# Optimization experiments

Hardware: AMD Instinct MI355X
Metric: run time of the kernel (lower is better)

Reference implementation:

```python
import jax, jax.numpy as jnp
import numpy as np

B, T, DIN, DOUT = 64, 128, 32, 64
HE, HD, K = 512, 1024, 12
NPH, NPL = 512, 64
# per-sample decoder parameter layout: Whh, bh, Wih, C, D
_PSI_SHAPES = [(HD, HD), (HD,), (DIN, HD), (HD, DOUT), (DIN, DOUT - DIN)]
_PSI_SIZES = [int(np.prod(s)) for s in _PSI_SHAPES]
_PSI_OFF = np.cumsum([0] + _PSI_SIZES)
NPSI = int(_PSI_OFF[-1])


def _xavier(key, shape):
    fan_in, fan_out = shape[-2], shape[-1]
    lim = np.sqrt(6.0 / (fan_in + fan_out))
    return jax.random.uniform(key, shape, jnp.float32, -lim, lim)


def setup_inputs() -> dict:
    key = jax.random.key(0)
    ks = jax.random.split(key, 16)
    gru_bias = jnp.concatenate([jnp.zeros(HD), jnp.ones(HD)])  # z-gate bias init to 1
    return {
        'inputs': jax.random.normal(ks[0], (B, T, DIN), jnp.float32),
        'outputs': jax.random.normal(ks[1], (B, T, DOUT), jnp.float32),
        'eps': jax.random.normal(ks[2], (B, K), jnp.float32),
        'state': jnp.zeros((B, HD), jnp.float32),
        'enc_Wih': _xavier(ks[3], (3 * HE, DOUT)),
        'enc_Whh': _xavier(ks[4], (3 * HE, HE)),
        'enc_bih': jnp.zeros(3 * HE, jnp.float32),
        'enc_bhh': jnp.zeros(3 * HE, jnp.float32),
        'to_mu': _xavier(ks[5], (HE, K)),
        'to_lsigma': _xavier(ks[6], (HE, K)),
        'to_lsigma_bias': -0.5 * jnp.ones(K, jnp.float32),
        'psi_W1': _xavier(ks[7], (K, NPH)),
        'psi_b1': jnp.zeros(NPH, jnp.float32),
        'psi_W2': _xavier(ks[8], (NPH, NPL)),
        'psi_b2': jnp.zeros(NPL, jnp.float32),
        'psi_W3': _xavier(ks[9], (NPL, NPSI)) * 0.05,
        'psi_b3': jnp.zeros(NPSI, jnp.float32),
        'gru_Wih': _xavier(ks[10], (DIN, 2 * HD)),
        'gru_Whh': _xavier(ks[11], (HD, 2 * HD)),
        'gru_bias': gru_bias,
    }


def _forward(inputs, outputs, eps, state, enc_Wih, enc_Whh, enc_bih, enc_bhh,
             to_mu, to_lsigma, to_lsigma_bias, psi_W1, psi_b1, psi_W2, psi_b2,
             psi_W3, psi_b3, gru_Wih, gru_Whh, gru_bias):
    # ---- encoder: shared GRUCell over time (torch GRUCell semantics) ----
    def enc_step(h, x):
        gi = x @ enc_Wih.T + enc_bih          # [B,3HE]
        gh = h @ enc_Whh.T + enc_bhh
        ir, iz, inn = jnp.split(gi, 3, axis=-1)
        hr, hz, hn = jnp.split(gh, 3, axis=-1)
        r = jax.nn.sigmoid(ir + hr)
        z = jax.nn.sigmoid(iz + hz)
        n = jnp.tanh(inn + r * hn)
        return (1.0 - z) * n + z * h, None
    h0 = jnp.zeros((outputs.shape[0], HE), outputs.dtype)
    h_enc, _ = jax.lax.scan(enc_step, h0, jnp.swapaxes(outputs, 0, 1))

    mu = h_enc @ to_mu
    logstd = h_enc @ to_lsigma + to_lsigma_bias
    z_lat = mu + eps * jnp.exp(logstd)

    # ---- hypernetwork: decode per-sample GRU params ----
    psi = (jnp.tanh(z_lat @ psi_W1 + psi_b1) @ psi_W2 + psi_b2) @ psi_W3 + psi_b3  # [B,NPSI]
    parts = [psi[:, _PSI_OFF[i]:_PSI_OFF[i + 1]].reshape((-1,) + _PSI_SHAPES[i])
             for i in range(5)]
    Whh_b, bh_b, Wih_b, C_b, D_b = parts

    # ---- per-sample partial GRU over time (batched via einsum) ----
    def dec_step(h, x):
        gx = x @ gru_Wih                       # [B,2HD] shared gates
        gh = h @ gru_Whh
        r = jax.nn.sigmoid(gx[:, :HD] + gh[:, :HD] + gru_bias[:HD])
        zt = jax.nn.sigmoid(gx[:, HD:] + gh[:, HD:] + gru_bias[HD:])
        eta = jnp.tanh(jnp.einsum('bi,bih->bh', x, Wih_b)
                       + r * jnp.einsum('bh,bhg->bg', h, Whh_b) + bh_b)
        h_new = zt * h + (1.0 - zt) * eta
        return h_new, h_new
    _, dec = jax.lax.scan(dec_step, state, jnp.swapaxes(inputs, 0, 1))
    dec = jnp.swapaxes(dec, 0, 1)              # [B,T,HD]

    # residual_output with HUMAN_SIZE > input_dim: concat(raw inputs, inputs@D)
    resid = jnp.concatenate([inputs, jnp.einsum('bti,bio->bto', inputs, D_b)], axis=-1)
    yhats = jnp.einsum('bth,bho->bto', dec, C_b) + resid
    states = jax.lax.stop_gradient(dec[:, -1, :])
    return yhats, mu, logstd, states


def reference(inputs, outputs, eps, state, enc_Wih, enc_Whh, enc_bih, enc_bhh,
              to_mu, to_lsigma, to_lsigma_bias, psi_W1, psi_b1, psi_W2, psi_b2,
              psi_W3, psi_b3, gru_Wih, gru_Whh, gru_bias):
    return _forward(inputs, outputs, eps, state, enc_Wih, enc_Whh, enc_bih, enc_bhh,
                    to_mu, to_lsigma, to_lsigma_bias, psi_W1, psi_b1, psi_W2, psi_b2,
                    psi_W3, psi_b3, gru_Wih, gru_Whh, gru_bias)
```

## Files before the change

kernel.cpp:

```cpp
#include <hip/hip_runtime.h>
#include <stdint.h>

#define B_ 64
#define T_ 128
#define DIN_ 32
#define DOUT_ 64
#define HE_ 512
#define HD_ 1024
#define NPSI_ 1148928
#define PPS_ 100352

typedef short bf16x8 __attribute__((ext_vector_type(8)));
typedef float f32x4 __attribute__((ext_vector_type(4)));
typedef int   i32x4 __attribute__((ext_vector_type(4)));

__device__ __forceinline__ unsigned short f2b(float f){
  unsigned u = __float_as_uint(f);
  u += 0x7fffu + ((u>>16)&1u);
  return (unsigned short)(u>>16);
}
__device__ __forceinline__ float b2f(unsigned short s){
  return __uint_as_float(((unsigned)s)<<16);
}
__device__ __forceinline__ float sigm_(float x){
  float e = __expf(-x);
  return 1.f/(1.f+e);
}
__device__ __forceinline__ float tanh_(float x){
  float e = __expf(2.f*x);
  return 1.f - 2.f/(e+1.f);
}
__device__ __forceinline__ void glds16(const void* g, void* l) {
  __builtin_amdgcn_global_load_lds(
      (const __attribute__((address_space(1))) unsigned int*)g,
      (__attribute__((address_space(3))) unsigned int*)l, 16, 0, 0);
}

__global__ __launch_bounds__(512) void k_prep(
    const float* __restrict__ enc_Whh, const float* __restrict__ enc_Wih,
    const float* __restrict__ gru_Whh, const float* __restrict__ state,
    unsigned short* __restrict__ encW_f, unsigned short* __restrict__ encI_f,
    unsigned short* __restrict__ gru_f, unsigned short* __restrict__ h_dec)
{
  int blk = blockIdx.x, tid = threadIdx.x;
  if (blk < 1536) {
    int nt = blk >> 4, kt = blk & 15;
    int c = tid >> 5, k = tid & 31;
    float v = enc_Whh[(size_t)(nt*16 + c)*HE_ + kt*32 + k];
    int l = c + ((k>>3)<<4), jj = k & 7;
    encW_f[(size_t)(nt*16 + kt)*512 + l*8 + jj] = f2b(v);
  } else if (blk < 1728) {
    int f = blk - 1536; int nt = f >> 1, kt = f & 1;
    int c = tid >> 5, k = tid & 31;
    float v = enc_Wih[(size_t)(nt*16 + c)*DOUT_ + kt*32 + k];
    int l = c + ((k>>3)<<4), jj = k & 7;
    encI_f[(size_t)(nt*2 + kt)*512 + l*8 + jj] = f2b(v);
  } else if (blk < 5824) {
    int f = blk - 1728; int nt = f >> 5, kt = f & 31;
    int k = tid >> 4, c = tid & 15;
    float v = gru_Whh[(size_t)(kt*32 + k)*2048 + nt*16 + c];
    int l = c + ((k>>3)<<4), jj = k & 7;
    gru_f[(size_t)(nt*32 + kt)*512 + l*8 + jj] = f2b(v);
  } else {
    int b = blk - 5824;
    h_dec[(size_t)b*HD_ + tid]       = f2b(state[(size_t)b*HD_ + tid]);
    h_dec[(size_t)b*HD_ + 512 + tid] = f2b(state[(size_t)b*HD_ + 512 + tid]);
  }
}

__global__ __launch_bounds__(128) void k_encoder(
    const float* __restrict__ outputs, const float* __restrict__ bih, const float* __restrict__ bhh,
    const unsigned short* __restrict__ encW_f, const unsigned short* __restrict__ encI_f,
    unsigned short* __restrict__ h_buf, float* __restrict__ h_enc, unsigned int* __restrict__ bar)
{
  __shared__ __align__(16) unsigned short h_bf[16*520];
  __shared__ __align__(16) unsigned short xa[16*72];
  __shared__ float part[64*16];
  int tid = threadIdx.x, wv = tid >> 6, lane = tid & 63;
  int g = blockIdx.x >> 5, bg = blockIdx.x & 31;
  int c0 = bg*16, gs = g*8;
  for (int i = tid; i < 16*520; i += 128) h_bf[i] = 0;
  for (int i = tid; i < 16*72; i += 128) xa[i] = 0;
  int cl = c0 + (lane & 15);
  float br_b = bih[cl] + bhh[cl];
  float bz_b = bih[512+cl] + bhh[512+cl];
  float bin_b = bih[1024+cl];
  float bhn_b = bhh[1024+cl];
  float hreg[4] = {0.f,0.f,0.f,0.f};
  int row = (lane>>4)<<2;
  int nt_r = bg, nt_z = 32+bg, nt_n = 64+bg;
  __syncthreads();
  for (int t = 0; t < 128; ++t) {
    int rb = t & 1;
    if (t > 0) {
      if (tid == 0) {
        while (__hip_atomic_load(&bar[(g<<7)+(t-1)], __ATOMIC_ACQUIRE, __HIP_MEMORY_SCOPE_AGENT) < 32u)
          __builtin_amdgcn_s_sleep(2);
      }
      __syncthreads();
    }
    {
      const unsigned short* src = h_buf + (size_t)rb*B_*HE_ + (size_t)gs*HE_;
      #pragma unroll
      for (int j = 0; j < 4; ++j) {
        int chunk = j*128 + tid;
        bf16x8 v = *(const bf16x8*)(src + chunk*8);
        int s = chunk >> 6, col = (chunk & 63) * 8;
        *(bf16x8*)(&h_bf[s*520 + col]) = v;
      }
      #pragma unroll
      for (int j = 0; j < 4; ++j) {
        int e = j*128 + tid;
        int s = e >> 6, d = e & 63;
        xa[s*72 + d] = f2b(outputs[((size_t)(gs+s)*T_ + t)*DOUT_ + d]);
      }
    }
    __syncthreads();
    f32x4 accr = {0,0,0,0}, accz = {0,0,0,0}, accn = {0,0,0,0}, accgi = {0,0,0,0};
    {
      bf16x8 a = *(const bf16x8*)(&xa[(lane&15)*72 + wv*32 + ((lane>>4)<<3)]);
      bf16x8 b0 = *(const bf16x8*)(encI_f + (size_t)(nt_r*2+wv)*512 + lane*8);
      bf16x8 b1 = *(const bf16x8*)(encI_f + (size_t)(nt_z*2+wv)*512 + lane*8);
      bf16x8 b2 = *(const bf16x8*)(encI_f + (size_t)(nt_n*2+wv)*512 + lane*8);
      accr  = __builtin_amdgcn_mfma_f32_16x16x32_bf16(a, b0, accr, 0,0,0);
      accz  = __builtin_amdgcn_mfma_f32_16x16x32_bf16(a, b1, accz, 0,0,0);
      accgi = __builtin_amdgcn_mfma_f32_16x16x32_bf16(a, b2, accgi, 0,0,0);
    }
    #pragma unroll
    for (int kk = 0; kk < 8; ++kk) {
      int kt = wv*8 + kk;
      bf16x8 a = *(const bf16x8*)(&h_bf[(lane&15)*520 + kt*32 + ((lane>>4)<<3)]);
      bf16x8 b0 = *(const bf16x8*)(encW_f + (size_t)(nt_r*16+kt)*512 + lane*8);
      bf16x8 b1 = *(const bf16x8*)(encW_f + (size_t)(nt_z*16+kt)*512 + lane*8);
      bf16x8 b2 = *(const bf16x8*)(encW_f + (size_t)(nt_n*16+kt)*512 + lane*8);
      accr = __builtin_amdgcn_mfma_f32_16x16x32_bf16(a, b0, accr, 0,0,0);
      accz = __builtin_amdgcn_mfma_f32_16x16x32_bf16(a, b1, accz, 0,0,0);
      accn = __builtin_amdgcn_mfma_f32_16x16x32_bf16(a, b2, accn, 0,0,0);
    }
    if (wv == 1) {
      #pragma unroll
      for (int i = 0; i < 4; ++i) {
        part[lane*16 + i]      = accr[i];
        part[lane*16 + 4 + i]  = accz[i];
        part[lane*16 + 8 + i]  = accn[i];
        part[lane*16 + 12 + i] = accgi[i];
      }
    }
    __syncthreads();
    if (wv == 0 && row < 8) {
      unsigned short* dst = h_buf + (size_t)(rb^1)*B_*HE_;
      #pragma unroll
      for (int i = 0; i < 4; ++i) {
        int s = row + i;
        float ar  = accr[i]  + part[lane*16 + i];
        float az  = accz[i]  + part[lane*16 + 4 + i];
        float an  = accn[i]  + part[lane*16 + 8 + i];
        float agi = accgi[i] + part[lane*16 + 12 + i];
        float r = sigm_(ar + br_b);
        float z = sigm_(az + bz_b);
        float n = tanh_(agi + bin_b + r*(an + bhn_b));
        float hn = (1.f - z)*n + z*hreg[i];
        hreg[i] = hn;
        dst[(size_t)(gs+s)*HE_ + cl] = f2b(hn);
        if (t == 127) h_enc[(size_t)(gs+s)*HE_ + cl] = hn;
      }
    }
    __syncthreads();
    if (tid == 0)
      __hip_atomic_fetch_add(&bar[(g<<7)+t], 1u, __ATOMIC_ACQ_REL, __HIP_MEMORY_SCOPE_AGENT);
  }
}

__global__ __launch_bounds__(64) void k_latent(
    const float* __restrict__ h_enc, const float* __restrict__ to_mu,
    const float* __restrict__ to_ls, const float* __restrict__ ls_bias,
    const float* __restrict__ eps, float* __restrict__ out_mu,
    float* __restrict__ out_ls, float* __restrict__ z_lat)
{
  __shared__ float hb[512];
  int b = blockIdx.x, tid = threadIdx.x;
  #pragma unroll
  for (int j = 0; j < 8; ++j) hb[j*64 + tid] = h_enc[(size_t)b*HE_ + j*64 + tid];
  __syncthreads();
  if (tid < 12) {
    float m = 0.f, s = 0.f;
    #pragma unroll 8
    for (int k = 0; k < 512; ++k) {
      float h = hb[k];
      m += h * to_mu[k*12 + tid];
      s += h * to_ls[k*12 + tid];
    }
    s += ls_bias[tid];
    out_mu[b*12 + tid] = m;
    out_ls[b*12 + tid] = s;
    z_lat[b*12 + tid] = m + eps[b*12 + tid] * __expf(s);
  }
}

__global__ __launch_bounds__(512) void k_hidden(
    const float* __restrict__ z_lat, const float* __restrict__ W1, const float* __restrict__ b1,
    const float* __restrict__ W2, const float* __restrict__ b2, float* __restrict__ hidden_T)
{
  __shared__ float zl[12];
  __shared__ float a[512];
  int b = blockIdx.x, tid = threadIdx.x;
  if (tid < 12) zl[tid] = z_lat[b*12 + tid];
  __syncthreads();
  float acc = b1[tid];
  #pragma unroll
  for (int k = 0; k < 12; ++k) acc += zl[k] * W1[k*512 + tid];
  a[tid] = tanh_(acc);
  __syncthreads();
  if (tid < 64) {
    float h = b2[tid];
    #pragma unroll 8
    for (int j = 0; j < 512; ++j) h += a[j] * W2[j*64 + tid];
    hidden_T[tid*64 + b] = h;
  }
}

__global__ __launch_bounds__(1024) void k_psi(
    const float* __restrict__ hidden_T, const float* __restrict__ W3, const float* __restrict__ b3,
    signed char* __restrict__ whh_q, float* __restrict__ scales, float* __restrict__ params)
{
  __shared__ float hid[64*64];
  __shared__ unsigned lmax[64];
  int tid = threadIdx.x, blk = blockIdx.x;
  if (tid < 64) lmax[tid] = 0;
  #pragma unroll
  for (int j = 0; j < 4; ++j) hid[j*1024 + tid] = hidden_T[j*1024 + tid];
  __syncthreads();
  float acc[64];
  size_t j; int i_loc = 0, c_loc = 0, kt = 0, cp = 0;
  bool is_whh = blk < 1024;
  if (is_whh) {
    kt = blk >> 5; cp = blk & 31;
    i_loc = tid >> 5; c_loc = tid & 31;
    j = (size_t)(kt*32 + i_loc)*1024 + cp*32 + c_loc;
  } else {
    j = (size_t)1048576 + (size_t)(blk - 1024)*1024 + tid;
  }
  float bv = b3[j];
  #pragma unroll
  for (int b = 0; b < 64; ++b) acc[b] = bv;
  for (int k = 0; k < 64; ++k) {
    float wv = W3[(size_t)k*NPSI_ + j];
    #pragma unroll
    for (int bq = 0; bq < 16; ++bq) {
      f32x4 h4 = *(const f32x4*)(&hid[k*64 + bq*4]);
      acc[bq*4+0] += wv * h4[0];
      acc[bq*4+1] += wv * h4[1];
      acc[bq*4+2] += wv * h4[2];
      acc[bq*4+3] += wv * h4[3];
    }
  }
  if (is_whh) {
    #pragma unroll
    for (int b = 0; b < 64; ++b)
      atomicMax(&lmax[b], __float_as_uint(fabsf(acc[b])));
    __syncthreads();
    int ct = cp*2 + (c_loc>>4);
    int l = (c_loc & 15) + (((i_loc>>3)&3)<<4);
    int jj = i_loc & 7;
    size_t base = ((size_t)ct*32 + (size_t)kt)*512 + l*8 + jj;
    #pragma unroll
    for (int b = 0; b < 64; ++b) {
      float m = __uint_as_float(lmax[b]);
      float inv = (m > 0.f) ? (127.f/m) : 0.f;
      int q = (int)rintf(acc[b]*inv);
      whh_q[(size_t)b*1048576 + base] = (signed char)q;
    }
    if (tid < 64)
      scales[(size_t)tid*1024 + kt*32 + cp] = __uint_as_float(lmax[tid]);
  } else {
    size_t off = j - 1048576;
    #pragma unroll
    for (int b = 0; b < 64; ++b)
      params[(size_t)b*PPS_ + off] = acc[b];
  }
}

__global__ __launch_bounds__(512, 2) void k_decoder(
    const float* __restrict__ inputs, const float* __restrict__ gru_Wih,
    const float* __restrict__ gru_bias,
    const signed char* __restrict__ whh_q, const float* __restrict__ scales,
    const unsigned short* __restrict__ gru_f, const float* __restrict__ params,
    unsigned short* __restrict__ h_buf, float* __restrict__ dec,
    float* __restrict__ out_states, unsigned int* __restrict__ bar)
{
  __shared__ __align__(16) unsigned short h_bf[8*1048];
  __shared__ __align__(16) signed char h_q8[8*1040];
  __shared__ __align__(16) char stg[8][2][6144];
  __shared__ unsigned short wih_lds[8192];
  __shared__ unsigned short gwih_lds[2048];
  __shared__ float x_lds[256];
  __shared__ float gh_lds[1024];
  __shared__ float mv_lds[256];
  __shared__ float sc_lds[256];
  int tid = threadIdx.x;
  int g = blockIdx.x >> 5, bg = blockIdx.x & 31;
  int c0 = bg*32, gs = g*8;
  int w = tid >> 6, lane = tid & 63;
  int s_t = (tid >> 5) & 7, c_t = tid & 31;
  int sg_t = gs + s_t, cg_t = c0 + c_t;
  float bh_r = 0.f, br_b = 0.f, bz_b = 0.f;
  if (tid < 256) {
    bh_r = params[(size_t)sg_t*PPS_ + cg_t];
    br_b = gru_bias[cg_t];
    bz_b = gru_bias[1024 + cg_t];
  }
  for (int idx = tid; idx < 2048; idx += 512) {
    int i = idx >> 6, gc = idx & 63;
    gwih_lds[idx] = f2b(gru_Wih[i*2048 + (gc>>5)*1024 + c0 + (gc&31)]);
  }
  for (int idx = tid; idx < 8192; idx += 512) {
    int s = idx >> 10, r = idx & 1023;
    wih_lds[idx] = f2b(params[(size_t)(gs+s)*PPS_ + 1024 + (r>>5)*1024 + c0 + (r&31)]);
  }
  if (lane < 32)
    sc_lds[w*32 + lane] = scales[(size_t)(gs+w)*1024 + lane*32 + bg] * (1.f/16129.f);
  const char* af0c = (const char*)whh_q + (size_t)((gs+w)*64 + 2*bg)*16384 + lane*16;
  const char* af1c = af0c + 16384;
  int j_t = w >> 1;
  int nt_j = (j_t < 2) ? (2*bg + j_t) : (64 + 2*bg + (j_t - 2));
  const char* gfc = (const char*)(gru_f + ((size_t)nt_j*32 + (w&1)*16)*512) + lane*16;
  int ho_l = (lane>>4)<<3;
  int ghk0 = (w&1)*16;
  char* bufA = &stg[w][0][0];
  char* bufB = &stg[w][1][0];

  auto ISSUE = [&](char* bufp, int cc) {
    const char* a0 = af0c + (size_t)cc*2048;
    const char* a1 = af1c + (size_t)cc*2048;
    const char* gg = gfc  + (size_t)cc*2048;
    glds16(a0,        bufp);        glds16(a0 + 1024, bufp + 1024);
    glds16(a1,        bufp + 2048); glds16(a1 + 1024, bufp + 3072);
    glds16(gg,        bufp + 4096); glds16(gg + 1024, bufp + 5120);
  };
  f32x4 agh, facc0, facc1;
  auto HALF = [&](char* bufp, int c) {
    asm volatile("s_waitcnt vmcnt(6)" ::: "memory");
    long a00 = *(const long*)(bufp + 0*512 + lane*8);
    long a01 = *(const long*)(bufp + 1*512 + lane*8);
    long a02 = *(const long*)(bufp + 2*512 + lane*8);
    long a03 = *(const long*)(bufp + 3*512 + lane*8);
    long a10 = *(const long*)(bufp + 2048 + 0*512 + lane*8);
    long a11 = *(const long*)(bufp + 2048 + 1*512 + lane*8);
    long a12 = *(const long*)(bufp + 2048 + 2*512 + lane*8);
    long a13 = *(const long*)(bufp + 2048 + 3*512 + lane*8);
    bf16x8 fg0 = *(const bf16x8*)(bufp + 4096 + lane*16);
    bf16x8 fg1 = *(const bf16x8*)(bufp + 5120 + lane*16);
    long hq0 = *(const long*)(h_q8 + w*1040 + (4*c+0)*32 + ho_l);
    long hq1 = *(const long*)(h_q8 + w*1040 + (4*c+1)*32 + ho_l);
    long hq2 = *(const long*)(h_q8 + w*1040 + (4*c+2)*32 + ho_l);
    long hq3 = *(const long*)(h_q8 + w*1040 + (4*c+3)*32 + ho_l);
    bf16x8 aA0 = *(const bf16x8*)(&h_bf[(lane&15)*1048 + (ghk0 + 2*c)*32 + ho_l]);
    bf16x8 aA1 = *(const bf16x8*)(&h_bf[(lane&15)*1048 + (ghk0 + 2*c+1)*32 + ho_l]);
    float s0 = sc_lds[w*32 + 4*c + 0];
    float s1 = sc_lds[w*32 + 4*c + 1];
    float s2 = sc_lds[w*32 + 4*c + 2];
    float s3 = sc_lds[w*32 + 4*c + 3];
    asm volatile("s_waitcnt lgkmcnt(0)" ::: "memory");
    __builtin_amdgcn_sched_barrier(0);
    ISSUE(bufp, (c + 2) & 7);
    i32x4 z4 = {0,0,0,0};
    i32x4 q;
    q = __builtin_amdgcn_mfma_i32_16x16x32_i8(a00, hq0, z4, 0,0,0);
    #pragma unroll
    for (int e = 0; e < 4; ++e) facc0[e] += (float)q[e]*s0;
    q = __builtin_amdgcn_mfma_i32_16x16x32_i8(a01, hq1, z4, 0,0,0);
    #pragma unroll
    for (int e = 0; e < 4; ++e) facc0[e] += (float)q[e]*s1;
    q = __builtin_amdgcn_mfma_i32_16x16x32_i8(a02, hq2, z4, 0,0,0);
    #pragma unroll
    for (int e = 0; e < 4; ++e) facc0[e] += (float)q[e]*s2;
    q = __builtin_amdgcn_mfma_i32_16x16x32_i8(a03, hq3, z4, 0,0,0);
    #pragma unroll
    for (int e = 0; e < 4; ++e) facc0[e] += (float)q[e]*s3;
    q = __builtin_amdgcn_mfma_i32_16x16x32_i8(a10, hq0, z4, 0,0,0);
    #pragma unroll
    for (int e = 0; e < 4; ++e) facc1[e] += (float)q[e]*s0;
    q = __builtin_amdgcn_mfma_i32_16x16x32_i8(a11, hq1, z4, 0,0,0);
    #pragma unroll
    for (int e = 0; e < 4; ++e) facc1[e] += (float)q[e]*s1;
    q = __builtin_amdgcn_mfma_i32_16x16x32_i8(a12, hq2, z4, 0,0,0);
    #pragma unroll
    for (int e = 0; e < 4; ++e) facc1[e] += (float)q[e]*s2;
    q = __builtin_amdgcn_mfma_i32_16x16x32_i8(a13, hq3, z4, 0,0,0);
    #pragma unroll
    for (int e = 0; e < 4; ++e) facc1[e] += (float)q[e]*s3;
    agh = __builtin_amdgcn_mfma_f32_16x16x32_bf16(aA0, fg0, agh, 0,0,0);
    agh = __builtin_amdgcn_mfma_f32_16x16x32_bf16(aA1, fg1, agh, 0,0,0);
  };

  __syncthreads();
  ISSUE(bufA, 0); ISSUE(bufB, 1);
  for (int t = 0; t < 128; ++t) {
    int rb = t & 1;
    if (t > 0 && tid == 0) {
      while (__hip_atomic_load(&bar[(g<<7)+(t-1)], __ATOMIC_ACQUIRE, __HIP_MEMORY_SCOPE_AGENT) < 32u)
        __builtin_amdgcn_s_sleep(1);
    }
    __builtin_amdgcn_s_barrier();
    {
      const char* hs = (const char*)(h_buf + (size_t)rb*B_*HD_ + (size_t)(gs + w)*HD_) + lane*16;
      glds16(hs,        &h_bf[w*1048]);
      glds16(hs + 1024, &h_bf[w*1048 + 512]);
    }
    if (tid < 256) x_lds[tid] = inputs[((size_t)sg_t*T_ + t)*DIN_ + c_t];
    asm volatile("s_waitcnt vmcnt(0)" ::: "memory");
    __builtin_amdgcn_s_barrier();
    {
      i32x4 pk;
      #pragma unroll
      for (int hh = 0; hh < 2; ++hh) {
        bf16x8 hv = *(const bf16x8*)(&h_bf[w*1048 + lane*16 + hh*8]);
        int lo = 0, hi2 = 0;
        #pragma unroll
        for (int e = 0; e < 4; ++e) {
          int q = (int)rintf(b2f((unsigned short)hv[e]) * 127.f);
          lo |= (q & 255) << (8*e);
        }
        #pragma unroll
        for (int e = 0; e < 4; ++e) {
          int q = (int)rintf(b2f((unsigned short)hv[4+e]) * 127.f);
          hi2 |= (q & 255) << (8*e);
        }
        pk[2*hh] = lo; pk[2*hh+1] = hi2;
      }
      *(i32x4*)(h_q8 + w*1040 + lane*16) = pk;
    }
    asm volatile("s_waitcnt lgkmcnt(0)" ::: "memory");
    agh = (f32x4){0,0,0,0}; facc0 = (f32x4){0,0,0,0}; facc1 = (f32x4){0,0,0,0};
    #pragma unroll 1
    for (int i2 = 0; i2 < 4; ++i2) {
      HALF(bufA, 2*i2);
      HALF(bufB, 2*i2 + 1);
    }
    if (lane < 32) {
      #pragma unroll
      for (int i = 0; i < 4; ++i)
        gh_lds[w*128 + ((lane>>4)*4 + i)*16 + (lane&15)] = agh[i];
    }
    if ((lane & 15) == 0) {
      int cb = (lane>>4)*4;
      #pragma unroll
      for (int i = 0; i < 4; ++i) {
        mv_lds[w*32 + cb + i]      = facc0[i];
        mv_lds[w*32 + 16 + cb + i] = facc1[i];
      }
    }
    asm volatile("s_waitcnt lgkmcnt(0)" ::: "memory");
    __builtin_amdgcn_s_barrier();
    if (tid < 256) {
      int jr = c_t >> 4, cl16 = c_t & 15;
      float ghr = gh_lds[(2*jr)*128   + s_t*16 + cl16] + gh_lds[(2*jr+1)*128 + s_t*16 + cl16];
      float ghz = gh_lds[(4+2*jr)*128 + s_t*16 + cl16] + gh_lds[(5+2*jr)*128 + s_t*16 + cl16];
      float gxr = 0.f, gxz = 0.f, ex = 0.f;
      #pragma unroll 8
      for (int i = 0; i < 32; ++i) {
        float xv = x_lds[s_t*32 + i];
        gxr += xv * b2f(gwih_lds[i*64 + c_t]);
        gxz += xv * b2f(gwih_lds[i*64 + 32 + c_t]);
        ex  += xv * b2f(wih_lds[s_t*1024 + i*32 + c_t]);
      }
      float r = sigm_(gxr + ghr + br_b);
      float z = sigm_(gxz + ghz + bz_b);
      float eta = tanh_(ex + bh_r + r * mv_lds[s_t*32 + c_t]);
      float ho_ = b2f(h_bf[s_t*1048 + c0 + c_t]);
      float hn = z*ho_ + (1.f - z)*eta;
      dec[((size_t)sg_t*T_ + t)*HD_ + cg_t] = hn;
      h_buf[(size_t)(rb^1)*B_*HD_ + (size_t)sg_t*HD_ + cg_t] = f2b(hn);
      if (t == 127) out_states[(size_t)sg_t*HD_ + cg_t] = hn;
    }
    asm volatile("s_waitcnt vmcnt(0)" ::: "memory");
    __builtin_amdgcn_s_barrier();
    if (t < 127 && tid == 0)
      __hip_atomic_fetch_add(&bar[(g<<7)+t], 1u, __ATOMIC_ACQ_REL, __HIP_MEMORY_SCOPE_AGENT);
  }
}

__global__ __launch_bounds__(256) void k_yhats(
    const float* __restrict__ dec, const float* __restrict__ inputs,
    const float* __restrict__ params, float* __restrict__ out_y)
{
  __shared__ __align__(16) float dsm[8*1024];
  __shared__ float xr[8*32];
  int blk = blockIdx.x, tid = threadIdx.x;
  int b = blk >> 4, t8 = (blk & 15) * 8;
  const float* prm = params + (size_t)b*PPS_;
  const float* C = prm + 33792;
  const float* D = prm + 99328;
  #pragma unroll
  for (int j = 0; j < 8; ++j) {
    int ch = j*256 + tid;
    *(f32x4*)(&dsm[ch*4]) = *(const f32x4*)(dec + ((size_t)b*T_ + t8)*HD_ + ch*4);
  }
  {
    int tl = tid >> 5, i = tid & 31;
    xr[tl*32 + i] = inputs[((size_t)b*T_ + t8 + tl)*DIN_ + i];
    xr[(tl+4)*32 + i] = inputs[((size_t)b*T_ + t8 + tl + 4)*DIN_ + i];
  }
  __syncthreads();
  int o = tid & 63;
  int tl0 = (tid >> 6) * 2;
  float a0 = 0.f, a1 = 0.f;
  #pragma unroll 4
  for (int h = 0; h < 1024; ++h) {
    float cv = C[h*64 + o];
    a0 += dsm[tl0*1024 + h] * cv;
    a1 += dsm[(tl0+1)*1024 + h] * cv;
  }
  float r0, r1;
  if (o < 32) {
    r0 = xr[tl0*32 + o];
    r1 = xr[(tl0+1)*32 + o];
  } else {
    r0 = 0.f; r1 = 0.f;
    #pragma unroll 8
    for (int i = 0; i < 32; ++i) {
      float dv = D[i*32 + (o-32)];
      r0 += xr[tl0*32 + i] * dv;
      r1 += xr[(tl0+1)*32 + i] * dv;
    }
  }
  out_y[((size_t)b*T_ + t8 + tl0)*DOUT_ + o]     = a0 + r0;
  out_y[((size_t)b*T_ + t8 + tl0 + 1)*DOUT_ + o] = a1 + r1;
}

extern "C" void kernel_launch(void* const* d_in, const int* in_sizes, int n_in,
                              void* d_out, int out_size, void* d_ws, size_t ws_size,
                              hipStream_t stream)
{
  const float* inputs  = (const float*)d_in[0];
  const float* outputs = (const float*)d_in[1];
  const float* eps     = (const float*)d_in[2];
  const float* state   = (const float*)d_in[3];
  const float* enc_Wih = (const float*)d_in[4];
  const float* enc_Whh = (const float*)d_in[5];
  const float* enc_bih = (const float*)d_in[6];
  const float* enc_bhh = (const float*)d_in[7];
  const float* to_mu   = (const float*)d_in[8];
  const float* to_ls   = (const float*)d_in[9];
  const float* to_lsb  = (const float*)d_in[10];
  const float* psi_W1  = (const float*)d_in[11];
  const float* psi_b1  = (const float*)d_in[12];
  const float* psi_W2  = (const float*)d_in[13];
  const float* psi_b2  = (const float*)d_in[14];
  const float* psi_W3  = (const float*)d_in[15];
  const float* psi_b3  = (const float*)d_in[16];
  const float* gru_Wih = (const float*)d_in[17];
  const float* gru_Whh = (const float*)d_in[18];
  const float* gru_bias= (const float*)d_in[19];
  float* out    = (float*)d_out;
  float* out_y  = out;
  float* out_mu = out + 524288;
  float* out_ls = out + 525056;
  float* out_st = out + 525824;

  if (ws_size < 135000000) return;
  char* ws = (char*)d_ws;
  size_t off = 0;
  auto alloc = [&](size_t bytes)->char*{ char* p = ws + off; off += (bytes + 255) & ~(size_t)255; return p; };
  signed char* whh_q      = (signed char*)alloc(67108864);
  float* scales           = (float*)alloc(262144);
  unsigned short* encW_f  = (unsigned short*)alloc(1572864);
  unsigned short* encI_f  = (unsigned short*)alloc(196608);
  unsigned short* gru_f   = (unsigned short*)alloc(4194304);
  float* params           = (float*)alloc(25690112);
  float* h_enc            = (float*)alloc(131072);
  float* z_lat            = (float*)alloc(3072);
  float* hidden_T         = (float*)alloc(16384);
  unsigned short* h_buf_e = (unsigned short*)alloc(131072);
  unsigned short* h_buf_d = (unsigned short*)alloc(262144);
  float* dec              = (float*)alloc(33554432);
  unsigned int* bar_e     = (unsigned int*)alloc(4096);
  unsigned int* bar_d     = (unsigned int*)alloc(8192);

  hipMemsetAsync(bar_e, 0, 4096, stream);
  hipMemsetAsync(bar_d, 0, 8192, stream);
  hipMemsetAsync(h_buf_e, 0, 131072, stream);

  k_prep<<<5888, 512, 0, stream>>>(enc_Whh, enc_Wih, gru_Whh, state, encW_f, encI_f, gru_f, h_buf_d);
  k_encoder<<<256, 128, 0, stream>>>(outputs, enc_bih, enc_bhh, encW_f, encI_f, h_buf_e, h_enc, bar_e);
  k_latent<<<64, 64, 0, stream>>>(h_enc, to_mu, to_ls, to_lsb, eps, out_mu, out_ls, z_lat);
  k_hidden<<<64, 512, 0, stream>>>(z_lat, psi_W1, psi_b1, psi_W2, psi_b2, hidden_T);
  k_psi<<<1122, 1024, 0, stream>>>(hidden_T, psi_W3, psi_b3, whh_q, scales, params);
  k_decoder<<<256, 512, 0, stream>>>(inputs, gru_Wih, gru_bias, whh_q, scales, gru_f, params, h_buf_d, dec, out_st, bar_d);
  k_yhats<<<1024, 256, 0, stream>>>(dec, inputs, params, out_y);
}
```

Measured before the change: 4.848 ms.

## Quantize shared GRU Whh to int8, split psi/encoder work, prefetch decoder across steps

The shared decoder GRU recurrent weights are now quantized to int8 with per-tile scales in k_prep and consumed through int8 MFMA in the decoder, which halves that stream's bytes. k_psi splits each Whh tile across two blocks by batch half and stages quantized output in LDS so global stores are coalesced. The encoder runs with 4 samples per group over 512 blocks instead of 8 over 256. The decoder remaps blockIdx so groups are interleaved and issues the first two weight chunks for the next timestep before the inter-block barrier. In exchange, int8 quantization of the shared weights adds accuracy risk, and the encoder now needs more atomic barrier traffic.

```diff
diff --git a/kernel.cpp b/kernel.cpp
--- a/kernel.cpp
+++ b/kernel.cpp
@@ -40,8 +40,11 @@
     const float* __restrict__ enc_Whh, const float* __restrict__ enc_Wih,
     const float* __restrict__ gru_Whh, const float* __restrict__ state,
     unsigned short* __restrict__ encW_f, unsigned short* __restrict__ encI_f,
-    unsigned short* __restrict__ gru_f, unsigned short* __restrict__ h_dec)
-{
+    signed char* __restrict__ gru_q, float* __restrict__ scales_g,
+    unsigned short* __restrict__ h_dec)
+{
+  __shared__ unsigned gmax_s;
+  __shared__ __align__(16) signed char gq[512];
   int blk = blockIdx.x, tid = threadIdx.x;
   if (blk < 1536) {
     int nt = blk >> 4, kt = blk & 15;
@@ -60,7 +63,20 @@
     int k = tid >> 4, c = tid & 15;
     float v = gru_Whh[(size_t)(kt*32 + k)*2048 + nt*16 + c];
     int l = c + ((k>>3)<<4), jj = k & 7;
-    gru_f[(size_t)(nt*32 + kt)*512 + l*8 + jj] = f2b(v);
+    if (tid == 0) gmax_s = 0;
+    __syncthreads();
+    float av = fabsf(v);
+    #pragma unroll
+    for (int d = 1; d < 64; d <<= 1) av = fmaxf(av, __shfl_xor(av, d));
+    if ((tid & 63) == 0) atomicMax(&gmax_s, __float_as_uint(av));
+    __syncthreads();
+    float m = __uint_as_float(gmax_s);
+    float inv = (m > 0.f) ? (127.f/m) : 0.f;
+    gq[l*8 + jj] = (signed char)(int)rintf(v*inv);
+    __syncthreads();
+    if (tid < 32)
+      *(i32x4*)(gru_q + (size_t)(nt*32 + kt)*512 + tid*16) = *(const i32x4*)(&gq[tid*16]);
+    if (tid == 0) scales_g[nt*32 + kt] = m;
   } else {
     int b = blk - 5824;
     h_dec[(size_t)b*HD_ + tid]       = f2b(state[(size_t)b*HD_ + tid]);
@@ -78,7 +94,7 @@
   __shared__ float part[64*16];
   int tid = threadIdx.x, wv = tid >> 6, lane = tid & 63;
   int g = blockIdx.x >> 5, bg = blockIdx.x & 31;
-  int c0 = bg*16, gs = g*8;
+  int c0 = bg*16, gs = g*4;
   for (int i = tid; i < 16*520; i += 128) h_bf[i] = 0;
   for (int i = tid; i < 16*72; i += 128) xa[i] = 0;
   int cl = c0 + (lane & 15);
@@ -87,7 +103,6 @@
   float bin_b = bih[1024+cl];
   float bhn_b = bhh[1024+cl];
   float hreg[4] = {0.f,0.f,0.f,0.f};
-  int row = (lane>>4)<<2;
   int nt_r = bg, nt_z = 32+bg, nt_n = 64+bg;
   __syncthreads();
   for (int t = 0; t < 128; ++t) {
@@ -102,14 +117,14 @@
     {
       const unsigned short* src = h_buf + (size_t)rb*B_*HE_ + (size_t)gs*HE_;
       #pragma unroll
-      for (int j = 0; j < 4; ++j) {
+      for (int j = 0; j < 2; ++j) {
         int chunk = j*128 + tid;
         bf16x8 v = *(const bf16x8*)(src + chunk*8);
         int s = chunk >> 6, col = (chunk & 63) * 8;
         *(bf16x8*)(&h_bf[s*520 + col]) = v;
       }
       #pragma unroll
-      for (int j = 0; j < 4; ++j) {
+      for (int j = 0; j < 2; ++j) {
         int e = j*128 + tid;
         int s = e >> 6, d = e & 63;
         xa[s*72 + d] = f2b(outputs[((size_t)(gs+s)*T_ + t)*DOUT_ + d]);
@@ -147,11 +162,11 @@
       }
     }
     __syncthreads();
-    if (wv == 0 && row < 8) {
+    if (wv == 0 && lane < 16) {
       unsigned short* dst = h_buf + (size_t)(rb^1)*B_*HE_;
       #pragma unroll
       for (int i = 0; i < 4; ++i) {
-        int s = row + i;
+        int s = i;
         float ar  = accr[i]  + part[lane*16 + i];
         float az  = accz[i]  + part[lane*16 + 4 + i];
         float an  = accn[i]  + part[lane*16 + 8 + i];
@@ -224,55 +239,79 @@
     signed char* __restrict__ whh_q, float* __restrict__ scales, float* __restrict__ params)
 {
   __shared__ float hid[64*64];
-  __shared__ unsigned lmax[64];
+  __shared__ unsigned lmax[32];
+  __shared__ __align__(16) signed char qtile[32*1024];
   int tid = threadIdx.x, blk = blockIdx.x;
-  if (tid < 64) lmax[tid] = 0;
+  if (tid < 32) lmax[tid] = 0;
   #pragma unroll
   for (int j = 0; j < 4; ++j) hid[j*1024 + tid] = hidden_T[j*1024 + tid];
   __syncthreads();
-  float acc[64];
-  size_t j; int i_loc = 0, c_loc = 0, kt = 0, cp = 0;
-  bool is_whh = blk < 1024;
+  bool is_whh = blk < 2048;
   if (is_whh) {
-    kt = blk >> 5; cp = blk & 31;
-    i_loc = tid >> 5; c_loc = tid & 31;
-    j = (size_t)(kt*32 + i_loc)*1024 + cp*32 + c_loc;
-  } else {
-    j = (size_t)1048576 + (size_t)(blk - 1024)*1024 + tid;
-  }
-  float bv = b3[j];
-  #pragma unroll
-  for (int b = 0; b < 64; ++b) acc[b] = bv;
-  for (int k = 0; k < 64; ++k) {
-    float wv = W3[(size_t)k*NPSI_ + j];
-    #pragma unroll
-    for (int bq = 0; bq < 16; ++bq) {
-      f32x4 h4 = *(const f32x4*)(&hid[k*64 + bq*4]);
-      acc[bq*4+0] += wv * h4[0];
-      acc[bq*4+1] += wv * h4[1];
-      acc[bq*4+2] += wv * h4[2];
-      acc[bq*4+3] += wv * h4[3];
-    }
-  }
-  if (is_whh) {
-    #pragma unroll
-    for (int b = 0; b < 64; ++b)
-      atomicMax(&lmax[b], __float_as_uint(fabsf(acc[b])));
-    __syncthreads();
-    int ct = cp*2 + (c_loc>>4);
+    int kt = blk >> 6, cp = (blk >> 1) & 31, bh = blk & 1;
+    int i_loc = tid >> 5, c_loc = tid & 31;
+    size_t j = (size_t)(kt*32 + i_loc)*1024 + cp*32 + c_loc;
+    float bv = b3[j];
+    float acc[32];
+    #pragma unroll
+    for (int b = 0; b < 32; ++b) acc[b] = bv;
+    for (int k = 0; k < 64; ++k) {
+      float wv = W3[(size_t)k*NPSI_ + j];
+      #pragma unroll
+      for (int bq = 0; bq < 8; ++bq) {
+        f32x4 h4 = *(const f32x4*)(&hid[k*64 + bh*32 + bq*4]);
+        acc[bq*4+0] += wv * h4[0];
+        acc[bq*4+1] += wv * h4[1];
+        acc[bq*4+2] += wv * h4[2];
+        acc[bq*4+3] += wv * h4[3];
+      }
+    }
+    #pragma unroll
+    for (int b = 0; b < 32; ++b) {
+      float av = fabsf(acc[b]);
+      #pragma unroll
+      for (int d = 1; d < 64; d <<= 1) av = fmaxf(av, __shfl_xor(av, d));
+      if ((tid & 63) == 0) atomicMax(&lmax[b], __float_as_uint(av));
+    }
+    __syncthreads();
     int l = (c_loc & 15) + (((i_loc>>3)&3)<<4);
     int jj = i_loc & 7;
-    size_t base = ((size_t)ct*32 + (size_t)kt)*512 + l*8 + jj;
-    #pragma unroll
-    for (int b = 0; b < 64; ++b) {
+    int base_lds = ((c_loc>>4)<<9) + l*8 + jj;
+    #pragma unroll
+    for (int b = 0; b < 32; ++b) {
       float m = __uint_as_float(lmax[b]);
       float inv = (m > 0.f) ? (127.f/m) : 0.f;
-      int q = (int)rintf(acc[b]*inv);
-      whh_q[(size_t)b*1048576 + base] = (signed char)q;
-    }
-    if (tid < 64)
-      scales[(size_t)tid*1024 + kt*32 + cp] = __uint_as_float(lmax[tid]);
+      qtile[b*1024 + base_lds] = (signed char)(int)rintf(acc[b]*inv);
+    }
+    __syncthreads();
+    #pragma unroll
+    for (int it = 0; it < 2; ++it) {
+      int qid = it*1024 + tid;
+      int b = qid >> 6, c64 = qid & 63;
+      i32x4 v = *(const i32x4*)(&qtile[b*1024 + c64*16]);
+      size_t goff = (size_t)(bh*32 + b)*1048576
+                  + (size_t)((2*cp + (c64>>5))*32 + kt)*512 + (c64&31)*16;
+      *(i32x4*)(whh_q + goff) = v;
+    }
+    if (tid < 32)
+      scales[(size_t)(bh*32 + tid)*1024 + kt*32 + cp] = __uint_as_float(lmax[tid]);
   } else {
+    size_t j = (size_t)1048576 + (size_t)(blk - 2048)*1024 + tid;
+    float bv = b3[j];
+    float acc[64];
+    #pragma unroll
+    for (int b = 0; b < 64; ++b) acc[b] = bv;
+    for (int k = 0; k < 64; ++k) {
+      float wv = W3[(size_t)k*NPSI_ + j];
+      #pragma unroll
+      for (int bq = 0; bq < 16; ++bq) {
+        f32x4 h4 = *(const f32x4*)(&hid[k*64 + bq*4]);
+        acc[bq*4+0] += wv * h4[0];
+        acc[bq*4+1] += wv * h4[1];
+        acc[bq*4+2] += wv * h4[2];
+        acc[bq*4+3] += wv * h4[3];
+      }
+    }
     size_t off = j - 1048576;
     #pragma unroll
     for (int b = 0; b < 64; ++b)
@@ -284,21 +323,24 @@
     const float* __restrict__ inputs, const float* __restrict__ gru_Wih,
     const float* __restrict__ gru_bias,
     const signed char* __restrict__ whh_q, const float* __restrict__ scales,
-    const unsigned short* __restrict__ gru_f, const float* __restrict__ params,
+    const signed char* __restrict__ gru_q, const float* __restrict__ scales_g,
+    const float* __restrict__ params,
     unsigned short* __restrict__ h_buf, float* __restrict__ dec,
     float* __restrict__ out_states, unsigned int* __restrict__ bar)
 {
   __shared__ __align__(16) unsigned short h_bf[8*1048];
   __shared__ __align__(16) signed char h_q8[8*1040];
-  __shared__ __align__(16) char stg[8][2][6144];
+  __shared__ __align__(16) char stg[8][2][5120];
   __shared__ unsigned short wih_lds[8192];
   __shared__ unsigned short gwih_lds[2048];
   __shared__ float x_lds[256];
   __shared__ float gh_lds[1024];
   __shared__ float mv_lds[256];
   __shared__ float sc_lds[256];
+  __shared__ float sgr_lds[128];
   int tid = threadIdx.x;
-  int g = blockIdx.x >> 5, bg = blockIdx.x & 31;
+  int i_b = blockIdx.x;
+  int g = (i_b >> 3) & 7, bg = (i_b & 7) + ((i_b >> 6) << 3);
   int c0 = bg*32, gs = g*8;
   int w = tid >> 6, lane = tid & 63;
   int s_t = (tid >> 5) & 7, c_t = tid & 31;
@@ -319,11 +361,13 @@
   }
   if (lane < 32)
     sc_lds[w*32 + lane] = scales[(size_t)(gs+w)*1024 + lane*32 + bg] * (1.f/16129.f);
+  int j_t = w >> 1;
+  int nt_j = (j_t < 2) ? (2*bg + j_t) : (64 + 2*bg + (j_t - 2));
+  if (lane < 16)
+    sgr_lds[w*16 + lane] = scales_g[nt_j*32 + (w&1)*16 + lane] * (1.f/16129.f);
   const char* af0c = (const char*)whh_q + (size_t)((gs+w)*64 + 2*bg)*16384 + lane*16;
   const char* af1c = af0c + 16384;
-  int j_t = w >> 1;
-  int nt_j = (j_t < 2) ? (2*bg + j_t) : (64 + 2*bg + (j_t - 2));
-  const char* gfc = (const char*)(gru_f + ((size_t)nt_j*32 + (w&1)*16)*512) + lane*16;
+  const char* gfc = (const char*)gru_q + ((size_t)nt_j*32 + (w&1)*16)*512 + lane*16;
   int ho_l = (lane>>4)<<3;
   int ghk0 = (w&1)*16;
   char* bufA = &stg[w][0][0];
@@ -332,14 +376,13 @@
   auto ISSUE = [&](char* bufp, int cc) {
     const char* a0 = af0c + (size_t)cc*2048;
     const char* a1 = af1c + (size_t)cc*2048;
-    const char* gg = gfc  + (size_t)cc*2048;
     glds16(a0,        bufp);        glds16(a0 + 1024, bufp + 1024);
     glds16(a1,        bufp + 2048); glds16(a1 + 1024, bufp + 3072);
-    glds16(gg,        bufp + 4096); glds16(gg + 1024, bufp + 5120);
+    glds16(gfc + (size_t)cc*1024, bufp + 4096);
   };
-  f32x4 agh, facc0, facc1;
-  auto HALF = [&](char* bufp, int c) {
-    asm volatile("s_waitcnt vmcnt(6)" ::: "memory");
+  f32x4 aghf, facc0, facc1;
+  auto HALF = [&](char* bufp, int c, int doIssue) {
+    asm volatile("s_waitcnt vmcnt(5)" ::: "memory");
     long a00 = *(const long*)(bufp + 0*512 + lane*8);
     long a01 = *(const long*)(bufp + 1*512 + lane*8);
     long a02 = *(const long*)(bufp + 2*512 + lane*8);
@@ -348,21 +391,22 @@
     long a11 = *(const long*)(bufp + 2048 + 1*512 + lane*8);
     long a12 = *(const long*)(bufp + 2048 + 2*512 + lane*8);
     long a13 = *(const long*)(bufp + 2048 + 3*512 + lane*8);
-    bf16x8 fg0 = *(const bf16x8*)(bufp + 4096 + lane*16);
-    bf16x8 fg1 = *(const bf16x8*)(bufp + 5120 + lane*16);
+    long qg0 = *(const long*)(bufp + 4096 + lane*8);
+    long qg1 = *(const long*)(bufp + 4608 + lane*8);
     long hq0 = *(const long*)(h_q8 + w*1040 + (4*c+0)*32 + ho_l);
     long hq1 = *(const long*)(h_q8 + w*1040 + (4*c+1)*32 + ho_l);
     long hq2 = *(const long*)(h_q8 + w*1040 + (4*c+2)*32 + ho_l);
     long hq3 = *(const long*)(h_q8 + w*1040 + (4*c+3)*32 + ho_l);
-    bf16x8 aA0 = *(const bf16x8*)(&h_bf[(lane&15)*1048 + (ghk0 + 2*c)*32 + ho_l]);
-    bf16x8 aA1 = *(const bf16x8*)(&h_bf[(lane&15)*1048 + (ghk0 + 2*c+1)*32 + ho_l]);
+    long haq0 = *(const long*)(h_q8 + (lane&15)*1040 + (ghk0 + 2*c)*32 + ho_l);
+    long haq1 = *(const long*)(h_q8 + (lane&15)*1040 + (ghk0 + 2*c+1)*32 + ho_l);
     float s0 = sc_lds[w*32 + 4*c + 0];
     float s1 = sc_lds[w*32 + 4*c + 1];
     float s2 = sc_lds[w*32 + 4*c + 2];
     float s3 = sc_lds[w*32 + 4*c + 3];
+    float g0 = sgr_lds[w*16 + 2*c], g1 = sgr_lds[w*16 + 2*c + 1];
     asm volatile("s_waitcnt lgkmcnt(0)" ::: "memory");
     __builtin_amdgcn_sched_barrier(0);
-    ISSUE(bufp, (c + 2) & 7);
+    if (doIssue) ISSUE(bufp, c + 2);
     i32x4 z4 = {0,0,0,0};
     i32x4 q;
     q = __builtin_amdgcn_mfma_i32_16x16x32_i8(a00, hq0, z4, 0,0,0);
@@ -389,8 +433,12 @@
     q = __builtin_amdgcn_mfma_i32_16x16x32_i8(a13, hq3, z4, 0,0,0);
     #pragma unroll
     for (int e = 0; e < 4; ++e) facc1[e] += (float)q[e]*s3;
-    agh = __builtin_amdgcn_mfma_f32_16x16x32_bf16(aA0, fg0, agh, 0,0,0);
-    agh = __builtin_amdgcn_mfma_f32_16x16x32_bf16(aA1, fg1, agh, 0,0,0);
+    q = __builtin_amdgcn_mfma_i32_16x16x32_i8(haq0, qg0, z4, 0,0,0);
+    #pragma unroll
+    for (int e = 0; e < 4; ++e) aghf[e] += (float)q[e]*g0;
+    q = __builtin_amdgcn_mfma_i32_16x16x32_i8(haq1, qg1, z4, 0,0,0);
+    #pragma unroll
+    for (int e = 0; e < 4; ++e) aghf[e] += (float)q[e]*g1;
   };
 
   __syncthreads();
@@ -431,16 +479,20 @@
       *(i32x4*)(h_q8 + w*1040 + lane*16) = pk;
     }
     asm volatile("s_waitcnt lgkmcnt(0)" ::: "memory");
-    agh = (f32x4){0,0,0,0}; facc0 = (f32x4){0,0,0,0}; facc1 = (f32x4){0,0,0,0};
+    __builtin_amdgcn_s_barrier();
+    aghf = (f32x4){0,0,0,0}; facc0 = (f32x4){0,0,0,0}; facc1 = (f32x4){0,0,0,0};
     #pragma unroll 1
-    for (int i2 = 0; i2 < 4; ++i2) {
-      HALF(bufA, 2*i2);
-      HALF(bufB, 2*i2 + 1);
-    }
+    for (int i2 = 0; i2 < 3; ++i2) {
+      HALF(bufA, 2*i2, 1);
+      HALF(bufB, 2*i2 + 1, 1);
+    }
+    HALF(bufA, 6, 0);
+    asm volatile("s_waitcnt vmcnt(0)" ::: "memory");
+    HALF(bufB, 7, 0);
     if (lane < 32) {
       #pragma unroll
       for (int i = 0; i < 4; ++i)
-        gh_lds[w*128 + ((lane>>4)*4 + i)*16 + (lane&15)] = agh[i];
+        gh_lds[w*128 + ((lane>>4)*4 + i)*16 + (lane&15)] = aghf[i];
     }
     if ((lane & 15) == 0) {
       int cb = (lane>>4)*4;
@@ -473,7 +525,12 @@
       h_buf[(size_t)(rb^1)*B_*HD_ + (size_t)sg_t*HD_ + cg_t] = f2b(hn);
       if (t == 127) out_states[(size_t)sg_t*HD_ + cg_t] = hn;
     }
-    asm volatile("s_waitcnt vmcnt(0)" ::: "memory");
+    if (t < 127) {
+      ISSUE(bufA, 0); ISSUE(bufB, 1);
+      asm volatile("s_waitcnt vmcnt(10)" ::: "memory");
+    } else {
+      asm volatile("s_waitcnt vmcnt(0)" ::: "memory");
+    }
     __builtin_amdgcn_s_barrier();
     if (t < 127 && tid == 0)
       __hip_atomic_fetch_add(&bar[(g<<7)+t], 1u, __ATOMIC_ACQ_REL, __HIP_MEMORY_SCOPE_AGENT);
@@ -558,7 +615,7 @@
   float* out_ls = out + 525056;
   float* out_st = out + 525824;
 
-  if (ws_size < 135000000) return;
+  if (ws_size < 130000000) return;
   char* ws = (char*)d_ws;
   size_t off = 0;
   auto alloc = [&](size_t bytes)->char*{ char* p = ws + off; off += (bytes + 255) & ~(size_t)255; return p; };
@@ -566,7 +623,8 @@
   float* scales           = (float*)alloc(262144);
   unsigned short* encW_f  = (unsigned short*)alloc(1572864);
   unsigned short* encI_f  = (unsigned short*)alloc(196608);
-  unsigned short* gru_f   = (unsigned short*)alloc(4194304);
+  signed char* gru_q      = (signed char*)alloc(2097152);
+  float* scales_g         = (float*)alloc(16384);
   float* params           = (float*)alloc(25690112);
   float* h_enc            = (float*)alloc(131072);
   float* z_lat            = (float*)alloc(3072);
@@ -574,18 +632,18 @@
   unsigned short* h_buf_e = (unsigned short*)alloc(131072);
   unsigned short* h_buf_d = (unsigned short*)alloc(262144);
   float* dec              = (float*)alloc(33554432);
-  unsigned int* bar_e     = (unsigned int*)alloc(4096);
+  unsigned int* bar_e     = (unsigned int*)alloc(8192);
   unsigned int* bar_d     = (unsigned int*)alloc(8192);
 
-  hipMemsetAsync(bar_e, 0, 4096, stream);
+  hipMemsetAsync(bar_e, 0, 8192, stream);
   hipMemsetAsync(bar_d, 0, 8192, stream);
   hipMemsetAsync(h_buf_e, 0, 131072, stream);
 
-  k_prep<<<5888, 512, 0, stream>>>(enc_Whh, enc_Wih, gru_Whh, state, encW_f, encI_f, gru_f, h_buf_d);
-  k_encoder<<<256, 128, 0, stream>>>(outputs, enc_bih, enc_bhh, encW_f, encI_f, h_buf_e, h_enc, bar_e);
+  k_prep<<<5888, 512, 0, stream>>>(enc_Whh, enc_Wih, gru_Whh, state, encW_f, encI_f, gru_q, scales_g, h_buf_d);
+  k_encoder<<<512, 128, 0, stream>>>(outputs, enc_bih, enc_bhh, encW_f, encI_f, h_buf_e, h_enc, bar_e);
   k_latent<<<64, 64, 0, stream>>>(h_enc, to_mu, to_ls, to_lsb, eps, out_mu, out_ls, z_lat);
   k_hidden<<<64, 512, 0, stream>>>(z_lat, psi_W1, psi_b1, psi_W2, psi_b2, hidden_T);
-  k_psi<<<1122, 1024, 0, stream>>>(hidden_T, psi_W3, psi_b3, whh_q, scales, params);
-  k_decoder<<<256, 512, 0, stream>>>(inputs, gru_Wih, gru_bias, whh_q, scales, gru_f, params, h_buf_d, dec, out_st, bar_d);
+  k_psi<<<2146, 1024, 0, stream>>>(hidden_T, psi_W3, psi_b3, whh_q, scales, params);
+  k_decoder<<<256, 512, 0, stream>>>(inputs, gru_Wih, gru_bias, whh_q, scales, gru_q, scales_g, params, h_buf_d, dec, out_st, bar_d);
   k_yhats<<<1024, 256, 0, stream>>>(dec, inputs, params, out_y);
 }
```

New measurement: 5.578 ms. 1.15x slower.
